# Performance work log

Measured on AMD Instinct MI355X. Metric: run time of the kernel, lower is better.

Reference implementation:

```python
import jax, jax.numpy as jnp
import numpy as np

N = 16384
DIMS = [3, 256, 256, 256, 256, 256, 256, 3]
NU = 1.0 / 100.0  # 1 / Reynold


def setup_inputs() -> dict:
    key = jax.random.key(0)
    ks = jax.random.split(key, 3 + 2 * (len(DIMS) - 1))
    inp = {
        "t": jax.random.uniform(ks[0], (N, 1), dtype=jnp.float32),
        "x": jax.random.uniform(ks[1], (N, 1), dtype=jnp.float32),
        "y": jax.random.uniform(ks[2], (N, 1), dtype=jnp.float32),
    }
    for i in range(len(DIMS) - 1):
        fan_in, fan_out = DIMS[i], DIMS[i + 1]
        # glorot_normal scale
        scale = jnp.sqrt(2.0 / (fan_in + fan_out)).astype(jnp.float32)
        inp[f"W{i}"] = jax.random.normal(ks[3 + 2 * i], (fan_in, fan_out), dtype=jnp.float32) * scale
        inp[f"b{i}"] = jax.random.normal(ks[4 + 2 * i], (fan_out,), dtype=jnp.float32) * 0.01
    return inp


def _mlp(p, params):
    # p: [3] single (t,x,y) point -> [3] (u,v,p)
    h = p
    for W, b in params[:-1]:
        h = jnp.sin(h @ W + b)
    W, b = params[-1]
    return h @ W + b


def reference(t, x, y, W0, b0, W1, b1, W2, b2, W3, b3, W4, b4, W5, b5, W6, b6):
    params = [(W0, b0), (W1, b1), (W2, b2), (W3, b3), (W4, b4), (W5, b5), (W6, b6)]
    f = lambda p: _mlp(p, params)
    txy = jnp.concatenate([t, x, y], axis=1)  # [N, 3]

    uvp = jax.vmap(f)(txy)                          # [N, 3]
    J = jax.vmap(jax.jacfwd(f))(txy)                # [N, 3(out), 3(in)]
    H = jax.vmap(jax.jacfwd(jax.jacfwd(f)))(txy)    # [N, 3(out), 3(in), 3(in)]

    u, v = uvp[:, 0], uvp[:, 1]
    u_t, u_x, u_y = J[:, 0, 0], J[:, 0, 1], J[:, 0, 2]
    v_t, v_x, v_y = J[:, 1, 0], J[:, 1, 1], J[:, 1, 2]
    p_x, p_y = J[:, 2, 1], J[:, 2, 2]
    u_xx, u_yy = H[:, 0, 1, 1], H[:, 0, 2, 2]
    v_xx, v_yy = H[:, 1, 1, 1], H[:, 1, 2, 2]

    eq1 = u_t + (u * u_x + v * u_y) + p_x - NU * (u_xx + u_yy)
    eq2 = v_t + (u * v_x + v * v_y) + p_y - NU * (v_xx + v_yy)
    eq3 = u_x + v_y
    return eq1[:, None], eq2[:, None], eq3[:, None]
```

## Files before the change

### kernel.cpp

```cpp
#include <hip/hip_runtime.h>

#define NPTS 16384
#define PW 32
#define NU (1.0f / 100.0f)

typedef _Float16 f16;
typedef __attribute__((ext_vector_type(8))) _Float16 f16x8;
typedef __attribute__((ext_vector_type(4))) float f32x4;

__device__ __forceinline__ int swz(int g) { return g ^ ((g >> 3) & 7); }

__global__ __launch_bounds__(256) void prep_kernel(
    const float* __restrict__ W1, const float* __restrict__ W2,
    const float* __restrict__ W3, const float* __restrict__ W4,
    const float* __restrict__ W5, const float* __restrict__ W6,
    f16* __restrict__ bh, f16* __restrict__ b6h)
{
    int idx = blockIdx.x * 256 + threadIdx.x;
    if (idx < 40960) {
        int col = idx & 255, subk = (idx >> 8) & 3, kc = (idx >> 10) & 7, L = idx >> 13;
        const float* W = (L == 0) ? W1 : (L == 1) ? W2 : (L == 2) ? W3 : (L == 3) ? W4 : W5;
        f16x8 vh;
        #pragma unroll
        for (int j = 0; j < 8; ++j) {
            int k = kc * 32 + subk * 8 + j;
            vh[j] = (f16)W[k * 256 + col];
        }
        int nf = col >> 4, l15 = col & 15, lane = subk * 16 + l15;
        *(f16x8*)(bh + (((L * 8 + kc) * 16 + nf) * 64 + lane) * 8) = vh;
    } else {
        int u = idx - 40960;
        if (u < 512) {
            int col = u & 15, subk = (u >> 4) & 3, kc = u >> 6;
            f16x8 vh;
            #pragma unroll
            for (int j = 0; j < 8; ++j) {
                int k = kc * 32 + subk * 8 + j;
                vh[j] = (f16)((col < 3) ? W6[k * 3 + col] : 0.f);
            }
            *(f16x8*)(b6h + (kc * 64 + subk * 16 + col) * 8) = vh;
        }
    }
}

__global__ __launch_bounds__(512, 2) void pinn_ns_mfma(
    const float* __restrict__ t_, const float* __restrict__ x_, const float* __restrict__ y_,
    const float* __restrict__ W0, const float* __restrict__ b0,
    const float* __restrict__ b1, const float* __restrict__ b2,
    const float* __restrict__ b3, const float* __restrict__ b4,
    const float* __restrict__ b5, const float* __restrict__ b6,
    const f16* __restrict__ bh, const f16* __restrict__ b6h,
    float* __restrict__ out)
{
    __shared__ __align__(16) f16 afrag[96 * 512];
    __shared__ float z6buf[6 * 32 * 4];

    const int tid = threadIdx.x;
    const int lane = tid & 63;
    const int wv = tid >> 6;
    const int pg = wv >> 2;
    const int nq = wv & 3;
    const int gl = swz(lane);
    const int p0 = blockIdx.x * PW;

    {
        int j = tid & 255, ph = tid >> 8;
        float wt = W0[j], wx = W0[256 + j], wy = W0[512 + j], bb0 = b0[j];
        int kc = j >> 5, sub = (j >> 3) & 3, jj = j & 7;
        #pragma unroll
        for (int pp = 0; pp < 16; ++pp) {
            int p = ph * 16 + pp;
            float tv = t_[p0 + p], xv = x_[p0 + p], yv = y_[p0 + p];
            float z = tv * wt + xv * wx + yv * wy + bb0;
            float sv, cv;
            __sincosf(z, &sv, &cv);
            float nv[6] = {sv, cv * wt, cv * wx, cv * wy, -sv * wx * wx, -sv * wy * wy};
            int g = swz(sub * 16 + pp);
            #pragma unroll
            for (int c = 0; c < 6; ++c)
                afrag[(((c * 2 + ph) * 8 + kc) * 64 + g) * 8 + jj] = (f16)nv[c];
        }
    }
    __syncthreads();

    const float* bias[5] = {b1, b2, b3, b4, b5};
    const f16x8* A = (const f16x8*)afrag;
    for (int L = 0; L < 5; ++L) {
        const f16x8* bH = (const f16x8*)bh + L * 8192;
        f32x4 acc[6][4];
        #pragma unroll
        for (int c = 0; c < 6; ++c)
            #pragma unroll
            for (int f = 0; f < 4; ++f)
                acc[c][f] = (f32x4){0.f, 0.f, 0.f, 0.f};

        f16x8 Bc[4];
        #pragma unroll
        for (int f = 0; f < 4; ++f)
            Bc[f] = bH[(nq * 4 + f) * 64 + lane];

        #pragma unroll
        for (int kc = 0; kc < 8; ++kc) {
            f16x8 Bn[4];
            if (kc < 7) {
                #pragma unroll
                for (int f = 0; f < 4; ++f)
                    Bn[f] = bH[((kc + 1) * 16 + nq * 4 + f) * 64 + lane];
            }
            #pragma unroll
            for (int c = 0; c < 6; ++c) {
                f16x8 Ah = A[((c * 2 + pg) * 8 + kc) * 64 + gl];
                #pragma unroll
                for (int f = 0; f < 4; ++f)
                    acc[c][f] = __builtin_amdgcn_mfma_f32_16x16x32_f16(Ah, Bc[f], acc[c][f], 0, 0, 0);
            }
            if (kc < 7) {
                #pragma unroll
                for (int f = 0; f < 4; ++f)
                    Bc[f] = Bn[f];
            }
        }
        __syncthreads();

        const float* bbp = bias[L];
        #pragma unroll
        for (int f = 0; f < 4; ++f) {
            int col = nq * 64 + f * 16 + (lane & 15);
            int kcw = col >> 5;
            int sub = (col >> 3) & 3, jj = col & 7;
            float bvf = bbp[col];
            #pragma unroll
            for (int r = 0; r < 4; ++r) {
                int rw = (lane >> 4) * 4 + r;
                float z = acc[0][f][r] + bvf;
                float zt = acc[1][f][r], zx = acc[2][f][r], zy = acc[3][f][r];
                float zxx = acc[4][f][r], zyy = acc[5][f][r];
                float sv, cv;
                __sincosf(z, &sv, &cv);
                float nv[6] = {sv, cv * zt, cv * zx, cv * zy,
                               cv * zxx - sv * zx * zx, cv * zyy - sv * zy * zy};
                int g = swz(sub * 16 + rw);
                #pragma unroll
                for (int c = 0; c < 6; ++c)
                    afrag[(((c * 2 + pg) * 8 + kcw) * 64 + g) * 8 + jj] = (f16)nv[c];
            }
        }
        __syncthreads();
    }

    if (wv < 6) {
        const f16x8* b6H = (const f16x8*)b6h;
        #pragma unroll
        for (int pgl = 0; pgl < 2; ++pgl) {
            f32x4 a6 = {0.f, 0.f, 0.f, 0.f};
            #pragma unroll
            for (int kc = 0; kc < 8; ++kc) {
                f16x8 Ah = A[((wv * 2 + pgl) * 8 + kc) * 64 + gl];
                a6 = __builtin_amdgcn_mfma_f32_16x16x32_f16(Ah, b6H[kc * 64 + lane], a6, 0, 0, 0);
            }
            int col = lane & 15;
            if (col < 3) {
                float badd = (wv == 0) ? b6[col] : 0.f;
                #pragma unroll
                for (int r = 0; r < 4; ++r)
                    z6buf[(wv * 32 + pgl * 16 + (lane >> 4) * 4 + r) * 4 + col] = a6[r] + badd;
            }
        }
    }
    __syncthreads();

    if (tid < PW) {
        int p = tid, g = p0 + p;
        float u_  = z6buf[(0   + p) * 4 + 0], v_  = z6buf[(0   + p) * 4 + 1];
        float ut  = z6buf[(32  + p) * 4 + 0], vt  = z6buf[(32  + p) * 4 + 1];
        float ux  = z6buf[(64  + p) * 4 + 0], vx  = z6buf[(64  + p) * 4 + 1], px = z6buf[(64 + p) * 4 + 2];
        float uy  = z6buf[(96  + p) * 4 + 0], vy  = z6buf[(96  + p) * 4 + 1], py = z6buf[(96 + p) * 4 + 2];
        float uxx = z6buf[(128 + p) * 4 + 0], vxx = z6buf[(128 + p) * 4 + 1];
        float uyy = z6buf[(160 + p) * 4 + 0], vyy = z6buf[(160 + p) * 4 + 1];
        out[g]            = ut + (u_ * ux + v_ * uy) + px - NU * (uxx + uyy);
        out[NPTS + g]     = vt + (u_ * vx + v_ * vy) + py - NU * (vxx + vyy);
        out[2 * NPTS + g] = ux + vy;
    }
}

extern "C" void kernel_launch(void* const* d_in, const int* in_sizes, int n_in,
                              void* d_out, int out_size, void* d_ws, size_t ws_size,
                              hipStream_t stream) {
    const float* t_ = (const float*)d_in[0];
    const float* x_ = (const float*)d_in[1];
    const float* y_ = (const float*)d_in[2];
    const float* W[7];
    const float* b[7];
    for (int i = 0; i < 7; ++i) {
        W[i] = (const float*)d_in[3 + 2 * i];
        b[i] = (const float*)d_in[4 + 2 * i];
    }
    float* out = (float*)d_out;

    f16* bh  = (f16*)d_ws;
    f16* b6h = bh + 5 * 65536;

    hipLaunchKernelGGL(prep_kernel, dim3(162), dim3(256), 0, stream,
                       W[1], W[2], W[3], W[4], W[5], W[6], bh, b6h);
    hipLaunchKernelGGL(pinn_ns_mfma, dim3(NPTS / PW), dim3(512), 0, stream,
                       t_, x_, y_, W[0], b[0],
                       b[1], b[2], b[3], b[4], b[5], b[6],
                       bh, b6h, out);
}
```

Baseline: 155.4 us.

## Halve points per block to 16 with 256-thread blocks

Reduces each block from 32 points and 8 waves to 16 points and 4 waves, removing the point-group split. LDS use per block halves, so more blocks can reside per CU and the grid doubles, which may improve scheduling and latency hiding. The trade-off is that each weight fragment loaded from global memory is reused across half as many points, so total weight traffic doubles.

```diff
diff --git a/kernel.cpp b/kernel.cpp
--- a/kernel.cpp
+++ b/kernel.cpp
@@ -1,7 +1,7 @@
 #include <hip/hip_runtime.h>
 
 #define NPTS 16384
-#define PW 32
+#define PW 16
 #define NU (1.0f / 100.0f)
 
 typedef _Float16 f16;
@@ -43,7 +43,7 @@
     }
 }
 
-__global__ __launch_bounds__(512, 2) void pinn_ns_mfma(
+__global__ __launch_bounds__(256, 3) void pinn_ns_mfma(
     const float* __restrict__ t_, const float* __restrict__ x_, const float* __restrict__ y_,
     const float* __restrict__ W0, const float* __restrict__ b0,
     const float* __restrict__ b1, const float* __restrict__ b2,
@@ -52,33 +52,30 @@
     const f16* __restrict__ bh, const f16* __restrict__ b6h,
     float* __restrict__ out)
 {
-    __shared__ __align__(16) f16 afrag[96 * 512];
-    __shared__ float z6buf[6 * 32 * 4];
+    __shared__ __align__(16) f16 afrag[6 * 8 * 512];
+    __shared__ float z6buf[6 * 16 * 4];
 
     const int tid = threadIdx.x;
     const int lane = tid & 63;
-    const int wv = tid >> 6;
-    const int pg = wv >> 2;
-    const int nq = wv & 3;
+    const int nq = tid >> 6;
     const int gl = swz(lane);
     const int p0 = blockIdx.x * PW;
 
     {
-        int j = tid & 255, ph = tid >> 8;
+        int j = tid;
         float wt = W0[j], wx = W0[256 + j], wy = W0[512 + j], bb0 = b0[j];
         int kc = j >> 5, sub = (j >> 3) & 3, jj = j & 7;
         #pragma unroll
-        for (int pp = 0; pp < 16; ++pp) {
-            int p = ph * 16 + pp;
+        for (int p = 0; p < PW; ++p) {
             float tv = t_[p0 + p], xv = x_[p0 + p], yv = y_[p0 + p];
             float z = tv * wt + xv * wx + yv * wy + bb0;
             float sv, cv;
             __sincosf(z, &sv, &cv);
             float nv[6] = {sv, cv * wt, cv * wx, cv * wy, -sv * wx * wx, -sv * wy * wy};
-            int g = swz(sub * 16 + pp);
+            int g = swz(sub * 16 + p);
             #pragma unroll
             for (int c = 0; c < 6; ++c)
-                afrag[(((c * 2 + ph) * 8 + kc) * 64 + g) * 8 + jj] = (f16)nv[c];
+                afrag[((c * 8 + kc) * 64 + g) * 8 + jj] = (f16)nv[c];
         }
     }
     __syncthreads();
@@ -109,7 +106,7 @@
             }
             #pragma unroll
             for (int c = 0; c < 6; ++c) {
-                f16x8 Ah = A[((c * 2 + pg) * 8 + kc) * 64 + gl];
+                f16x8 Ah = A[(c * 8 + kc) * 64 + gl];
                 #pragma unroll
                 for (int f = 0; f < 4; ++f)
                     acc[c][f] = __builtin_amdgcn_mfma_f32_16x16x32_f16(Ah, Bc[f], acc[c][f], 0, 0, 0);
@@ -142,41 +139,38 @@
                 int g = swz(sub * 16 + rw);
                 #pragma unroll
                 for (int c = 0; c < 6; ++c)
-                    afrag[(((c * 2 + pg) * 8 + kcw) * 64 + g) * 8 + jj] = (f16)nv[c];
+                    afrag[((c * 8 + kcw) * 64 + g) * 8 + jj] = (f16)nv[c];
             }
         }
         __syncthreads();
     }
 
-    if (wv < 6) {
+    for (int cc = nq; cc < 6; cc += 4) {
+        f32x4 a6 = {0.f, 0.f, 0.f, 0.f};
         const f16x8* b6H = (const f16x8*)b6h;
         #pragma unroll
-        for (int pgl = 0; pgl < 2; ++pgl) {
-            f32x4 a6 = {0.f, 0.f, 0.f, 0.f};
-            #pragma unroll
-            for (int kc = 0; kc < 8; ++kc) {
-                f16x8 Ah = A[((wv * 2 + pgl) * 8 + kc) * 64 + gl];
-                a6 = __builtin_amdgcn_mfma_f32_16x16x32_f16(Ah, b6H[kc * 64 + lane], a6, 0, 0, 0);
-            }
-            int col = lane & 15;
-            if (col < 3) {
-                float badd = (wv == 0) ? b6[col] : 0.f;
-                #pragma unroll
-                for (int r = 0; r < 4; ++r)
-                    z6buf[(wv * 32 + pgl * 16 + (lane >> 4) * 4 + r) * 4 + col] = a6[r] + badd;
-            }
+        for (int kc = 0; kc < 8; ++kc) {
+            f16x8 Ah = A[(cc * 8 + kc) * 64 + gl];
+            a6 = __builtin_amdgcn_mfma_f32_16x16x32_f16(Ah, b6H[kc * 64 + lane], a6, 0, 0, 0);
+        }
+        int col = lane & 15;
+        if (col < 3) {
+            float badd = (cc == 0) ? b6[col] : 0.f;
+            #pragma unroll
+            for (int r = 0; r < 4; ++r)
+                z6buf[(cc * 16 + (lane >> 4) * 4 + r) * 4 + col] = a6[r] + badd;
         }
     }
     __syncthreads();
 
     if (tid < PW) {
         int p = tid, g = p0 + p;
-        float u_  = z6buf[(0   + p) * 4 + 0], v_  = z6buf[(0   + p) * 4 + 1];
-        float ut  = z6buf[(32  + p) * 4 + 0], vt  = z6buf[(32  + p) * 4 + 1];
-        float ux  = z6buf[(64  + p) * 4 + 0], vx  = z6buf[(64  + p) * 4 + 1], px = z6buf[(64 + p) * 4 + 2];
-        float uy  = z6buf[(96  + p) * 4 + 0], vy  = z6buf[(96  + p) * 4 + 1], py = z6buf[(96 + p) * 4 + 2];
-        float uxx = z6buf[(128 + p) * 4 + 0], vxx = z6buf[(128 + p) * 4 + 1];
-        float uyy = z6buf[(160 + p) * 4 + 0], vyy = z6buf[(160 + p) * 4 + 1];
+        float u_  = z6buf[(0  + p) * 4 + 0], v_  = z6buf[(0  + p) * 4 + 1];
+        float ut  = z6buf[(16 + p) * 4 + 0], vt  = z6buf[(16 + p) * 4 + 1];
+        float ux  = z6buf[(32 + p) * 4 + 0], vx  = z6buf[(32 + p) * 4 + 1], px = z6buf[(32 + p) * 4 + 2];
+        float uy  = z6buf[(48 + p) * 4 + 0], vy  = z6buf[(48 + p) * 4 + 1], py = z6buf[(48 + p) * 4 + 2];
+        float uxx = z6buf[(64 + p) * 4 + 0], vxx = z6buf[(64 + p) * 4 + 1];
+        float uyy = z6buf[(80 + p) * 4 + 0], vyy = z6buf[(80 + p) * 4 + 1];
         out[g]            = ut + (u_ * ux + v_ * uy) + px - NU * (uxx + uyy);
         out[NPTS + g]     = vt + (u_ * vx + v_ * vy) + py - NU * (vxx + vyy);
         out[2 * NPTS + g] = ux + vy;
@@ -202,7 +196,7 @@
 
     hipLaunchKernelGGL(prep_kernel, dim3(162), dim3(256), 0, stream,
                        W[1], W[2], W[3], W[4], W[5], W[6], bh, b6h);
-    hipLaunchKernelGGL(pinn_ns_mfma, dim3(NPTS / PW), dim3(512), 0, stream,
+    hipLaunchKernelGGL(pinn_ns_mfma, dim3(NPTS / PW), dim3(256), 0, stream,
                        t_, x_, y_, W[0], b[0],
                        b[1], b[2], b[3], b[4], b[5], b[6],
                        bh, b6h, out);
```

Result: slower. 239.8 us (+54.3%).
